# Optimization experiments

Hardware: AMD Instinct MI355X
Metric: run time of the kernel (lower is better)

The kernel has to match this reference:

```python
import jax, jax.numpy as jnp
import numpy as np

N, C, H, W = 8, 128, 56, 56
CO = C // 8  # 16


def setup_inputs() -> dict:
    key = jax.random.key(0)
    k1, k2, k3, k4 = jax.random.split(key, 4)
    x = jax.random.normal(k1, (N, C, H, W), dtype=jnp.float32)
    # p_3: Conv2d(c*35 -> c//8, 1x1). The unfold channel order is (c, kh=5, kw=7),
    # so the 1x1 conv over c*35 channels is exactly a dilated 5x7 conv with
    # weight [CO, C, 5, 7] and rhs_dilation (2, 3).
    w3 = jax.random.normal(k2, (CO, C, 5, 7), dtype=jnp.float32) * 0.02
    w4 = jax.random.normal(k3, (CO, CO), dtype=jnp.float32) * 0.1
    w5 = jax.random.normal(k4, (C, CO), dtype=jnp.float32) * 0.1
    return {"x": x, "w3": w3, "w4": w4, "w5": w5}


def reference(x, w3, w4, w5):
    # Fused equivalent of: unfold(5x1, dil 2, pad 4) -> unfold(1x7, dil 3, pad 9)
    # -> 1x1 conv (c*35 -> c//8). Padding (4,4)/(9,9) keeps 'same' spatial size.
    y = jax.lax.conv_general_dilated(
        x, w3,
        window_strides=(1, 1),
        padding=((4, 4), (9, 9)),
        rhs_dilation=(2, 3),
        dimension_numbers=("NCHW", "OIHW", "NCHW"),
    )  # [N, CO, H, W]
    y = jnp.einsum("oc,nchw->nohw", w4, y)  # p_4: 1x1 conv CO->CO
    y = jnp.einsum("oc,nchw->nohw", w5, y)  # p_5: 1x1 conv CO->C
    return y
```

## Files before the change

### kernel.cpp

```cpp
#include <hip/hip_runtime.h>

#define BN 8
#define BC 128
#define BH 56
#define BW 56
#define HW 3136
#define NTAP 35
#define WS_WC 71680
#define WS_XP (WS_WC + 4096)
#define XROW 2368

typedef unsigned short u16;
typedef unsigned int u32;
typedef __bf16 bf16x8 __attribute__((ext_vector_type(8)));
typedef float f32x4 __attribute__((ext_vector_type(4)));

__device__ __forceinline__ u16 f2b(float f) {
    unsigned u = __float_as_uint(f);
    return (u16)((u + 0x7FFFu + ((u >> 16) & 1u)) >> 16);
}
__device__ __forceinline__ u32 pack2(float a, float b) {
    return (u32)f2b(a) | ((u32)f2b(b) << 16);
}
__device__ __forceinline__ void dma16(const void* g, void* l) {
    __builtin_amdgcn_global_load_lds(
        (const __attribute__((address_space(1))) u32*)g,
        (__attribute__((address_space(3))) u32*)l, 16, 0, 0);
}

__global__ __launch_bounds__(256) void prep_all(
    const float* __restrict__ x, const float* __restrict__ w3,
    const float* __restrict__ w4, const float* __restrict__ w5,
    u16* __restrict__ ws)
{
    const int b = blockIdx.x;
    const int tid = threadIdx.x;

    if (b >= 2048) {
        int i = (b - 2048) * 256 + tid;
        if (i < WS_WC) {
            int j = i & 7, lane = (i >> 3) & 63, r = i >> 9;
            int tap = r % NTAP, cc = r / NTAP;
            int q = lane >> 4, lm = lane & 15;
            ws[i] = f2b(w3[(lm * BC + cc * 32 + q * 8 + j) * NTAP + tap]);
        } else if (i < WS_WC + 4096) {
            int i2 = i - WS_WC;
            int j = i2 & 7, lane = (i2 >> 3) & 63, ot = i2 >> 9;
            int q = lane >> 4, lm = lane & 15, o = ot * 16 + lm, k = q * 8 + j;
            float s = 0.f;
            if (k < 16)
                for (int c = 0; c < 16; ++c) s += w5[o * 16 + c] * w4[c * 16 + k];
            ws[i] = f2b(s);
        }
        return;
    }

    __shared__ float ls[32][57];
    const int hp = b & 63, cc = (b >> 6) & 3, n = b >> 8;
    u32* dst = (u32*)(ws + WS_XP + (size_t)((n * 4 + cc) * 64 + hp) * XROW);
    const int gr = hp - 4;

    if ((unsigned)gr >= BH) {
        for (int i = tid; i < XROW / 2; i += 256) dst[i] = 0u;
        return;
    }
    for (int i = tid; i < 32 * 14; i += 256) {
        int c = i / 14, w4i = i % 14;
        float4 v = *(const float4*)(x + ((size_t)(n * BC + cc * 32 + c) * BH + gr) * BW + 4 * w4i);
        ls[c][4 * w4i + 0] = v.x;
        ls[c][4 * w4i + 1] = v.y;
        ls[c][4 * w4i + 2] = v.z;
        ls[c][4 * w4i + 3] = v.w;
    }
    __syncthreads();
    for (int i = tid; i < 74 * 16; i += 256) {
        int col = i >> 4, cp = i & 15;
        int gw = col - 9;
        u32 v = 0u;
        if ((unsigned)gw < BW) v = pack2(ls[2 * cp][gw], ls[2 * cp + 1][gw]);
        dst[col * 16 + cp] = v;
    }
}

__global__ __launch_bounds__(512, 4) void conv_mfma(
    const u16* __restrict__ wsT, float* __restrict__ out)
{
    __shared__ __align__(16) u16 xs[5][74][32];
    __shared__ __align__(16) u16 y3T[32][40];
    __shared__ __align__(16) float cbuf[2][3][64][4];

    const int n = blockIdx.x & 7;
    const int r0 = blockIdx.x >> 3;
    const int h = r0 >> 1, wh = r0 & 1;
    const int tid = threadIdx.x, lane = tid & 63, wv = tid >> 6;
    const int wt = wv >> 2, g = wv & 3;
    const int q = lane >> 4, lm = lane & 15;
    const int wl = wt * 16 + lm;
    const int wg = wh * 28 + wl;
    const bool wok = (wl < 28);

    if (tid < 256) ((u32*)&y3T[tid >> 3][16])[tid & 7] = 0u;

    f32x4 acc = {0.f, 0.f, 0.f, 0.f};
    char* xsf = (char*)&xs[0][0][0];
    const int t0 = 9 * g;
    const int ntap = (g == 3) ? 8 : 9;

    for (int cc = 0; cc < 4; ++cc) {
        __syncthreads();

        const u16* xbase = wsT + WS_XP + (size_t)((n * 4 + cc) * 64 + h) * XROW;
        for (int k = wv; k < 24; k += 8) {
            int bb = k * 1024 + lane * 16;
            int r = bb / 4736;
            int off = bb - r * 4736;
            if (k < 23 || lane < 8)
                dma16(xbase + (size_t)(2 * r) * XROW + (off >> 1), xsf + bb);
        }
        __syncthreads();

        const u16* wbase = wsT + (size_t)cc * NTAP * 512 + (size_t)lane * 8;
        bf16x8 areg[9];
        #pragma unroll
        for (int tt = 0; tt < 9; ++tt) {
            int t = t0 + tt;
            int tc = (t < NTAP) ? t : (NTAP - 1);
            areg[tt] = *(const bf16x8*)(wbase + (size_t)tc * 512);
        }
        #pragma unroll
        for (int tt = 0; tt < 9; ++tt) {
            if (tt < ntap) {
                int t = t0 + tt;
                int kh = t / 7, kw = t - 7 * kh;
                bf16x8 b = *(const bf16x8*)&xs[kh][wg + 3 * kw][q * 8];
                acc = __builtin_amdgcn_mfma_f32_16x16x32_bf16(areg[tt], b, acc, 0, 0, 0);
            }
        }
    }

    if (g > 0) {
        cbuf[wt][g - 1][lane][0] = acc[0];
        cbuf[wt][g - 1][lane][1] = acc[1];
        cbuf[wt][g - 1][lane][2] = acc[2];
        cbuf[wt][g - 1][lane][3] = acc[3];
    }
    __syncthreads();
    if (g == 0) {
        #pragma unroll
        for (int p = 0; p < 3; ++p) {
            acc[0] += cbuf[wt][p][lane][0];
            acc[1] += cbuf[wt][p][lane][1];
            acc[2] += cbuf[wt][p][lane][2];
            acc[3] += cbuf[wt][p][lane][3];
        }
        u32 lo = wok ? pack2(acc[0], acc[1]) : 0u;
        u32 hi = wok ? pack2(acc[2], acc[3]) : 0u;
        *(u32*)&y3T[wl][q * 4]     = lo;
        *(u32*)&y3T[wl][q * 4 + 2] = hi;
    }
    __syncthreads();

    bf16x8 bfrag = *(const bf16x8*)&y3T[wl][q * 8];
    #pragma unroll
    for (int i = 0; i < 2; ++i) {
        const int ot = 2 * g + i;
        bf16x8 afrag = *(const bf16x8*)(wsT + WS_WC + (size_t)(ot * 64 + lane) * 8);
        f32x4 c2 = {0.f, 0.f, 0.f, 0.f};
        c2 = __builtin_amdgcn_mfma_f32_16x16x32_bf16(afrag, bfrag, c2, 0, 0, 0);
        if (wok) {
            int o = ot * 16 + q * 4;
            float* po = out + ((size_t)(n * BC + o) * BH + h) * BW + wg;
            po[0]      = c2[0];
            po[HW]     = c2[1];
            po[2 * HW] = c2[2];
            po[3 * HW] = c2[3];
        }
    }
}

extern "C" void kernel_launch(void* const* d_in, const int* in_sizes, int n_in,
                              void* d_out, int out_size, void* d_ws, size_t ws_size,
                              hipStream_t stream)
{
    (void)in_sizes; (void)n_in; (void)out_size; (void)ws_size;
    const float* x  = (const float*)d_in[0];
    const float* w3 = (const float*)d_in[1];
    const float* w4 = (const float*)d_in[2];
    const float* w5 = (const float*)d_in[3];
    u16* ws = (u16*)d_ws;

    prep_all<<<2048 + 296, 256, 0, stream>>>(x, w3, w4, w5, ws);
    conv_mfma<<<BN * BH * 2, 512, 0, stream>>>(ws, (float*)d_out);
}
```

Baseline: 92.36 us.

## Stage conv weights in LDS via DMA and trim input tile to half-row

Each block now DMAs only the 48 input columns its half-row needs, instead of the full padded 74-column row. It also DMAs all 35 tap weight fragments for the current channel chunk into LDS, replacing the per-wave global register loads. The reduction buffer is aliased onto the input tile region, and the launch bound occupancy hint goes from 4 to 6. The aim is to cut global load traffic and register pressure, at the cost of a larger total LDS footprint that may limit how many blocks fit per CU.

```diff
diff --git a/kernel.cpp b/kernel.cpp
--- a/kernel.cpp
+++ b/kernel.cpp
@@ -9,6 +9,10 @@
 #define WS_WC 71680
 #define WS_XP (WS_WC + 4096)
 #define XROW 2368
+#define XS_OFF 0
+#define Y3_OFF 15360
+#define WA_OFF 17920
+#define SMEM_SZ 53760
 
 typedef unsigned short u16;
 typedef unsigned int u32;
@@ -82,12 +86,14 @@
     }
 }
 
-__global__ __launch_bounds__(512, 4) void conv_mfma(
+__global__ __launch_bounds__(512, 6) void conv_mfma(
     const u16* __restrict__ wsT, float* __restrict__ out)
 {
-    __shared__ __align__(16) u16 xs[5][74][32];
-    __shared__ __align__(16) u16 y3T[32][40];
-    __shared__ __align__(16) float cbuf[2][3][64][4];
+    __shared__ __align__(16) char smem[SMEM_SZ];
+    u16* xs  = (u16*)(smem + XS_OFF);
+    u16* y3T = (u16*)(smem + Y3_OFF);
+    u16* wA  = (u16*)(smem + WA_OFF);
+    float* cbuf = (float*)(smem + XS_OFF);
 
     const int n = blockIdx.x & 7;
     const int r0 = blockIdx.x >> 3;
@@ -99,68 +105,61 @@
     const int wg = wh * 28 + wl;
     const bool wok = (wl < 28);
 
-    if (tid < 256) ((u32*)&y3T[tid >> 3][16])[tid & 7] = 0u;
+    if (tid < 256) ((u32*)(y3T + (tid >> 3) * 40))[8 + (tid & 7)] = 0u;
 
     f32x4 acc = {0.f, 0.f, 0.f, 0.f};
-    char* xsf = (char*)&xs[0][0][0];
     const int t0 = 9 * g;
     const int ntap = (g == 3) ? 8 : 9;
 
     for (int cc = 0; cc < 4; ++cc) {
         __syncthreads();
 
-        const u16* xbase = wsT + WS_XP + (size_t)((n * 4 + cc) * 64 + h) * XROW;
-        for (int k = wv; k < 24; k += 8) {
-            int bb = k * 1024 + lane * 16;
-            int r = bb / 4736;
-            int off = bb - r * 4736;
-            if (k < 23 || lane < 8)
-                dma16(xbase + (size_t)(2 * r) * XROW + (off >> 1), xsf + bb);
+        const u16* xbase = wsT + WS_XP + (size_t)((n * 4 + cc) * 64 + h) * XROW
+                         + wh * 28 * 32;
+        for (int k = wv; k < 15; k += 8) {
+            int r = k / 3, s = k - 3 * r;
+            dma16(xbase + (size_t)(2 * r) * XROW + s * 512 + lane * 8,
+                  smem + XS_OFF + r * 3072 + s * 1024 + lane * 16);
         }
+        const u16* wbase = wsT + (size_t)cc * NTAP * 512;
+        for (int k = wv; k < NTAP; k += 8)
+            dma16(wbase + (size_t)k * 512 + lane * 8,
+                  smem + WA_OFF + k * 1024 + lane * 16);
+
         __syncthreads();
 
-        const u16* wbase = wsT + (size_t)cc * NTAP * 512 + (size_t)lane * 8;
-        bf16x8 areg[9];
-        #pragma unroll
-        for (int tt = 0; tt < 9; ++tt) {
-            int t = t0 + tt;
-            int tc = (t < NTAP) ? t : (NTAP - 1);
-            areg[tt] = *(const bf16x8*)(wbase + (size_t)tc * 512);
-        }
         #pragma unroll
         for (int tt = 0; tt < 9; ++tt) {
             if (tt < ntap) {
                 int t = t0 + tt;
                 int kh = t / 7, kw = t - 7 * kh;
-                bf16x8 b = *(const bf16x8*)&xs[kh][wg + 3 * kw][q * 8];
-                acc = __builtin_amdgcn_mfma_f32_16x16x32_bf16(areg[tt], b, acc, 0, 0, 0);
+                bf16x8 a = *(const bf16x8*)(wA + (size_t)(t * 64 + lane) * 8);
+                bf16x8 b = *(const bf16x8*)(xs + ((kh * 48 + wl + 3 * kw) * 32 + q * 8));
+                acc = __builtin_amdgcn_mfma_f32_16x16x32_bf16(a, b, acc, 0, 0, 0);
             }
         }
     }
 
+    __syncthreads();
     if (g > 0) {
-        cbuf[wt][g - 1][lane][0] = acc[0];
-        cbuf[wt][g - 1][lane][1] = acc[1];
-        cbuf[wt][g - 1][lane][2] = acc[2];
-        cbuf[wt][g - 1][lane][3] = acc[3];
+        float* cb = cbuf + ((wt * 3 + (g - 1)) * 64 + lane) * 4;
+        cb[0] = acc[0]; cb[1] = acc[1]; cb[2] = acc[2]; cb[3] = acc[3];
     }
     __syncthreads();
     if (g == 0) {
         #pragma unroll
         for (int p = 0; p < 3; ++p) {
-            acc[0] += cbuf[wt][p][lane][0];
-            acc[1] += cbuf[wt][p][lane][1];
-            acc[2] += cbuf[wt][p][lane][2];
-            acc[3] += cbuf[wt][p][lane][3];
+            const float* cb = cbuf + ((wt * 3 + p) * 64 + lane) * 4;
+            acc[0] += cb[0]; acc[1] += cb[1]; acc[2] += cb[2]; acc[3] += cb[3];
         }
         u32 lo = wok ? pack2(acc[0], acc[1]) : 0u;
         u32 hi = wok ? pack2(acc[2], acc[3]) : 0u;
-        *(u32*)&y3T[wl][q * 4]     = lo;
-        *(u32*)&y3T[wl][q * 4 + 2] = hi;
+        *(u32*)(y3T + wl * 40 + q * 4)     = lo;
+        *(u32*)(y3T + wl * 40 + q * 4 + 2) = hi;
     }
     __syncthreads();
 
-    bf16x8 bfrag = *(const bf16x8*)&y3T[wl][q * 8];
+    bf16x8 bfrag = *(const bf16x8*)(y3T + wl * 40 + q * 8);
     #pragma unroll
     for (int i = 0; i < 2; ++i) {
         const int ot = 2 * g + i;
```

Measured after the change: 89.97 us. 1.03x faster.
